# Optimization experiments

Hardware: AMD Instinct MI355X
Metric: run time of the kernel (lower is better)

Reference implementation:

```python
import jax, jax.numpy as jnp
import numpy as np

D = 512      # input_dim == encoder d_model
E = 512      # embedding_dim (codebook dim)
V = 8192     # num_embeddings
NC = 1       # num_codebooks
L = 6        # encoder layers
H = 8        # heads
F = 2048     # ffn dim
HD = D // H
EPS = 1e-5


def layernorm(x, s, b):
    m = jnp.mean(x, -1, keepdims=True)
    v = jnp.mean((x - m) ** 2, -1, keepdims=True)
    return (x - m) * jax.lax.rsqrt(v + EPS) * s + b


def sinusoidal_pe(T):
    pos = np.arange(T, dtype=np.float32)[:, None]
    i = np.arange(0, D, 2, dtype=np.float32)[None, :]
    ang = pos / np.power(10000.0, i / D)
    pe = np.zeros((T, D), np.float32)
    pe[:, 0::2] = np.sin(ang)
    pe[:, 1::2] = np.cos(ang)
    return jnp.asarray(pe)


def setup_inputs():
    key = jax.random.key(0)
    ks = jax.random.split(key, 12)
    B, T = 8, 1024
    xs = jax.random.normal(ks[0], (B, T, D), jnp.float32)
    xs_lens = (T // 2 + jax.random.randint(ks[1], (B,), 0, T // 2)).astype(jnp.int32)
    mask_indices = jax.random.uniform(ks[2], (B, T)) < 0.12  # span-mask surrogate
    sc = lambda k, shape, s=0.02: jax.random.normal(k, shape, jnp.float32) * s
    return {
        "xs": xs, "xs_lens": xs_lens, "mask_indices": mask_indices,
        "W_embed": sc(ks[3], (D, D), D ** -0.5),
        "ln1_s": jnp.ones((L, D)), "ln1_b": jnp.zeros((L, D)),
        "Wqkv": sc(ks[4], (L, D, 3 * D)), "Wo": sc(ks[5], (L, D, D)),
        "ln2_s": jnp.ones((L, D)), "ln2_b": jnp.zeros((L, D)),
        "W1": sc(ks[6], (L, D, F)), "W2": sc(ks[7], (L, F, D)),
        "an_s": jnp.ones((D,)), "an_b": jnp.zeros((D,)),
        "iln_s": jnp.ones((D,)), "iln_b": jnp.zeros((D,)),
        "mask_emb": sc(ks[8], (D,), 0.1),
        "top_n_out": sc(ks[9], (NC, D, V)),
        "projection": sc(ks[10], (D, E), (2.0 / (D + E)) ** 0.5),  # xavier_normal, frozen
        "embeddings": jax.random.normal(ks[11], (NC, E, V), jnp.float32),  # frozen codebook
    }


def encoder_blocks(x, pad_mask, ln1_s, ln1_b, Wqkv, Wo, ln2_s, ln2_b, W1, W2, an_s, an_b):
    B, T, _ = x.shape
    attn_bias = jnp.where(pad_mask, 0.0, -1e9)[:, None, None, :]  # [B,1,1,T]

    def layer(x, p):
        l1s, l1b, wqkv, wo, l2s, l2b, w1, w2 = p
        h = layernorm(x, l1s, l1b)
        q, k, v = jnp.split(h @ wqkv, 3, axis=-1)
        q = q.reshape(B, T, H, HD)
        k = k.reshape(B, T, H, HD)
        v = v.reshape(B, T, H, HD)
        scores = jnp.einsum('bqhd,bkhd->bhqk', q, k) * (HD ** -0.5) + attn_bias
        o = jnp.einsum('bhqk,bkhd->bqhd', jax.nn.softmax(scores, axis=-1), v)
        x = x + o.reshape(B, T, D) @ wo
        h = layernorm(x, l2s, l2b)
        x = x + jax.nn.relu(h @ w1) @ w2
        return x, None

    x, _ = jax.lax.scan(layer, x, (ln1_s, ln1_b, Wqkv, Wo, ln2_s, ln2_b, W1, W2))
    return layernorm(x, an_s, an_b)


def nearest_ids(x, iln_s, iln_b, projection, embeddings):
    # layernorm -> projection -> squared-distance argmin per codebook
    B, T, _ = x.shape
    z = layernorm(x, iln_s, iln_b) @ projection        # [B,T,E]
    flat = z.reshape(-1, E)                            # [N,E]
    d = (jnp.sum(flat ** 2, 1)[None, :, None]
         + jnp.sum(embeddings ** 2, 1)[:, None, :]
         - 2.0 * jnp.einsum('ne,gev->gnv', flat, embeddings))  # [NC,N,V]
    return jnp.argmin(d, -1).T.reshape(B, T, NC)


def reference(xs, xs_lens, mask_indices, W_embed, ln1_s, ln1_b, Wqkv, Wo, ln2_s, ln2_b,
              W1, W2, an_s, an_b, iln_s, iln_b, mask_emb, top_n_out, projection, embeddings):
    B, T, _ = xs.shape
    pad_mask = jnp.arange(T)[None, :] < xs_lens[:, None]              # [B,T]
    x = xs @ W_embed + sinusoidal_pe(T)[None]                         # encoder.embed
    target_ids = nearest_ids(x, iln_s, iln_b, projection, embeddings)  # [B,T,NC]
    masked_xs = jnp.where(mask_indices[..., None], mask_emb, x)
    out = encoder_blocks(masked_xs, pad_mask, ln1_s, ln1_b, Wqkv, Wo,
                         ln2_s, ln2_b, W1, W2, an_s, an_b)            # [B,T,D]
    logits = jnp.einsum('btd,gdv->bgtv', out, top_n_out)              # [B,NC,T,V]
    lsm = jax.nn.log_softmax(logits, axis=-1)
    tgt = jnp.transpose(target_ids, (0, 2, 1))                        # [B,NC,T]
    ent = -jnp.take_along_axis(lsm, tgt[..., None], axis=-1)[..., 0]  # [B,NC,T]
    m = (pad_mask & mask_indices).astype(jnp.float32)                 # [B,T]
    loss = jnp.sum(ent * m[:, None, :]) / (jnp.sum(m) * NC)
    return loss
```

## Files before the change

### kernel.cpp

```cpp
#include <hip/hip_runtime.h>
#include <hip/hip_bf16.h>

#define D_ 512
#define T_ 1024
#define B_ 8
#define H_ 8
#define F_ 2048
#define V_ 8192
#define L_ 6
#define NTOK 8192
#define EPS_ 1e-5f
#define NCAP 2048

typedef short short8 __attribute__((ext_vector_type(8)));
typedef float floatx4 __attribute__((ext_vector_type(4)));

__device__ __forceinline__ float bf2f(unsigned short u) {
  union { unsigned int i; float f; } v; v.i = ((unsigned int)u) << 16; return v.f;
}
__device__ __forceinline__ unsigned short f2bf(float f) {
  unsigned int u = __float_as_uint(f);
  return (unsigned short)((u + 0x7fffu + ((u >> 16) & 1u)) >> 16);
}
__device__ __forceinline__ float ldf(const void* p, long long i, int bf) {
  if (bf) return bf2f(((const unsigned short*)p)[i]);
  return ((const float*)p)[i];
}
__device__ __forceinline__ void ld16(const unsigned short* g, unsigned short* l) {
  __builtin_amdgcn_global_load_lds(
      (const __attribute__((address_space(1))) unsigned int*)g,
      (__attribute__((address_space(3))) unsigned int*)l, 16, 0, 0);
}
__device__ __forceinline__ unsigned int fkey(float f) {
  unsigned int u = __float_as_uint(f);
  return (u & 0x80000000u) ? ~u : (u ^ 0x80000000u);
}

__global__ void detect_kernel(const unsigned int* xsw, const unsigned int* mw, int* flags) {
  __shared__ int cnt[256];
  __shared__ int m01[256], mlo[256], mhi[256];
  int tid = threadIdx.x;
  int c = 0;
  for (int t = tid; t < 1024; t += 256) {
    unsigned int lo = xsw[t] & 0xffffu;
    int ok;
    if (lo == 0u) ok = 1;
    else { unsigned int e = (lo >> 7) & 0xffu; ok = (e >= 90u && e <= 140u); }
    c += ok;
  }
  int n01 = 0, lo38 = 0, hi38 = 0;
  for (int t = tid; t < 2048; t += 256) {
    unsigned int w = mw[t];
    if (w > 1u) n01 = 1;
    if ((w & 0xffffu) == 0x3f80u) lo38 = 1;
    if ((w >> 16) == 0x3f80u) hi38 = 1;
  }
  cnt[tid] = c; m01[tid] = n01; mlo[tid] = lo38; mhi[tid] = hi38;
  __syncthreads();
  for (int s = 128; s > 0; s >>= 1) {
    if (tid < s) {
      cnt[tid] += cnt[tid + s];
      m01[tid] |= m01[tid + s]; mlo[tid] |= mlo[tid + s]; mhi[tid] |= mhi[tid + s];
    }
    __syncthreads();
  }
  if (tid == 0) {
    flags[0] = (cnt[0] > 700) ? 1 : 0;
    int fmt;
    if (!m01[0]) fmt = 0;
    else if (mlo[0]) fmt = 2;
    else if (mhi[0]) fmt = 3;
    else fmt = 1;
    flags[1] = fmt;
  }
}

__global__ void conv_all_kernel(const void* d4, const void* d5, const void* d8,
                                const void* d9, const void* d12, const void* d13,
                                const void* d14, const void* d15, const void* d16,
                                float* P, const int* flags) {
  int i = blockIdx.x * 256 + threadIdx.x;
  if (i >= 14848) return;
  int bf = flags[0];
  const void* src; int off;
  if (i < 3072) { src = d4; off = 0; }
  else if (i < 6144) { src = d5; off = 3072; }
  else if (i < 9216) { src = d8; off = 6144; }
  else if (i < 12288) { src = d9; off = 9216; }
  else if (i < 12800) { src = d12; off = 12288; }
  else if (i < 13312) { src = d13; off = 12800; }
  else if (i < 13824) { src = d14; off = 13312; }
  else if (i < 14336) { src = d15; off = 13824; }
  else { src = d16; off = 14336; }
  P[i] = ldf(src, i - off, bf);
}

__global__ void convb_kernel(const void* src, unsigned short* dst, int n, const int* flags) {
  int i = blockIdx.x * 256 + threadIdx.x;
  if (i < n) {
    if (flags[0]) dst[i] = ((const unsigned short*)src)[i];
    else dst[i] = f2bf(((const float*)src)[i]);
  }
}

__global__ __launch_bounds__(256) void trans_kernel(const void* src, unsigned short* dst,
                                                    int K, int N, const int* flags) {
  int bf = flags[0];
  __shared__ unsigned short tile[32][33];
  int n0 = blockIdx.x * 32, k0 = blockIdx.y * 32, batch = blockIdx.z;
  long long sbase = (long long)batch * K * N;
  long long dbase = (long long)batch * N * K;
  int c = threadIdx.x & 31, r8 = threadIdx.x >> 5;
#pragma unroll
  for (int rr = 0; rr < 4; ++rr) {
    int r = r8 + rr * 8;
    tile[r][c] = f2bf(ldf(src, sbase + (long long)(k0 + r) * N + n0 + c, bf));
  }
  __syncthreads();
#pragma unroll
  for (int rr = 0; rr < 4; ++rr) {
    int nn = r8 + rr * 8;
    dst[dbase + (long long)(n0 + nn) * K + k0 + c] = tile[c][nn];
  }
}

__global__ __launch_bounds__(256) void trans_big_kernel(const void* top, const void* emb,
                                                        unsigned short* TOPT, unsigned short* EMBT,
                                                        float* en, const int* flags) {
  int bf = flags[0];
  __shared__ unsigned short tile[32][33];
  int n0 = blockIdx.x * 32, k0 = blockIdx.y * 32, z = blockIdx.z;
  const void* src = z ? emb : top;
  unsigned short* dst = z ? EMBT : TOPT;
  int c = threadIdx.x & 31, r8 = threadIdx.x >> 5;
#pragma unroll
  for (int rr = 0; rr < 4; ++rr) {
    int r = r8 + rr * 8;
    tile[r][c] = f2bf(ldf(src, (long long)(k0 + r) * V_ + n0 + c, bf));
  }
  __syncthreads();
#pragma unroll
  for (int rr = 0; rr < 4; ++rr) {
    int nn = r8 + rr * 8;
    dst[(long long)(n0 + nn) * D_ + k0 + c] = tile[c][nn];
  }
  if (z == 1 && threadIdx.x < 32) {
    int nn = threadIdx.x;
    float s = 0.f;
#pragma unroll
    for (int r = 0; r < 32; ++r) { float x = bf2f(tile[r][nn]); s += x * x; }
    atomicAdd(&en[n0 + nn], s);
  }
}

__global__ void prep_kernel(const void* mask, const int* lens, int* maski, float* mcomb,
                            int* idx, int* cnt, const int* flags) {
  int i = blockIdx.x * 256 + threadIdx.x;
  if (i >= NTOK) return;
  int fmt = flags[1];
  int mi;
  if (fmt == 0) mi = ((const int*)mask)[i] != 0;
  else if (fmt == 1) mi = ((const unsigned char*)mask)[i] != 0;
  else if (fmt == 2) mi = ((const unsigned short*)mask)[i] != 0;
  else mi = ((const float*)mask)[i] != 0.f;
  int b = i >> 10, t = i & (T_ - 1);
  int act = mi && (t < lens[b]);
  maski[i] = mi;
  mcomb[i] = act ? 1.f : 0.f;
  if (act) {
    int p = atomicAdd(cnt, 1);
    if (p < NCAP) idx[p] = i;
  }
}

#define BK 32
__device__ __forceinline__ void mfma_core(const unsigned short* A, const unsigned short* BT,
                                          int m0, int n0, int Kdim,
                                          unsigned short (*As)[BK], unsigned short (*Bs)[BK],
                                          floatx4 acc[4][4], int tid) {
  int wave = tid >> 6, lane = tid & 63;
  int r16 = lane >> 2, c16 = lane & 3;
  int lrow = lane & 15, quad = lane >> 4;
  int wm = (wave & 1) * 64, wn = (wave >> 1) * 64;
  for (int k0 = 0; k0 < Kdim; k0 += BK) {
#pragma unroll
    for (int p = 0; p < 2; ++p) {
      int rr = wave * 32 + p * 16;
      ld16(A + (long long)(m0 + rr + r16) * Kdim + k0 + c16 * 8, &As[rr][0]);
      ld16(BT + (long long)(n0 + rr + r16) * Kdim + k0 + c16 * 8, &Bs[rr][0]);
    }
    __syncthreads();
    short8 af[4], bfr[4];
#pragma unroll
    for (int i = 0; i < 4; ++i) af[i] = *(const short8*)&As[wm + i * 16 + lrow][quad * 8];
#pragma unroll
    for (int j = 0; j < 4; ++j) bfr[j] = *(const short8*)&Bs[wn + j * 16 + lrow][quad * 8];
#pragma unroll
    for (int i = 0; i < 4; ++i)
#pragma unroll
      for (int j = 0; j < 4; ++j)
        acc[i][j] = __builtin_amdgcn_mfma_f32_16x16x32_bf16(af[i], bfr[j], acc[i][j], 0, 0, 0);
    __syncthreads();
  }
}

__device__ __forceinline__ void mfma_core_g(const unsigned short* A, const int* ridx,
                                            const unsigned short* BT, int m0, int n0,
                                            unsigned short (*As)[BK], unsigned short (*Bs)[BK],
                                            floatx4 acc[4][4], int tid) {
  int wave = tid >> 6, lane = tid & 63;
  int r16 = lane >> 2, c16 = lane & 3;
  int lrow = lane & 15, quad = lane >> 4;
  int wm = (wave & 1) * 64, wn = (wave >> 1) * 64;
  int ar0 = ridx[m0 + wave * 32 + r16];
  int ar1 = ridx[m0 + wave * 32 + 16 + r16];
  for (int k0 = 0; k0 < D_; k0 += BK) {
    ld16(A + (long long)ar0 * D_ + k0 + c16 * 8, &As[wave * 32][0]);
    ld16(A + (long long)ar1 * D_ + k0 + c16 * 8, &As[wave * 32 + 16][0]);
#pragma unroll
    for (int p = 0; p < 2; ++p) {
      int rr = wave * 32 + p * 16;
      ld16(BT + (long long)(n0 + rr + r16) * D_ + k0 + c16 * 8, &Bs[rr][0]);
    }
    __syncthreads();
    short8 af[4], bfr[4];
#pragma unroll
    for (int i = 0; i < 4; ++i) af[i] = *(const short8*)&As[wm + i * 16 + lrow][quad * 8];
#pragma unroll
    for (int j = 0; j < 4; ++j) bfr[j] = *(const short8*)&Bs[wn + j * 16 + lrow][quad * 8];
#pragma unroll
    for (int i = 0; i < 4; ++i)
#pragma unroll
      for (int j = 0; j < 4; ++j)
        acc[i][j] = __builtin_amdgcn_mfma_f32_16x16x32_bf16(af[i], bfr[j], acc[i][j], 0, 0, 0);
    __syncthreads();
  }
}

__global__ __launch_bounds__(256) void mgemm_kernel(const unsigned short* A,
    const unsigned short* BT, long long boff, unsigned short* Cb, int Ndim, int Kdim) {
  __shared__ __align__(16) unsigned short As[128][BK];
  __shared__ __align__(16) unsigned short Bs[128][BK];
  int tid = threadIdx.x;
  int bid = blockIdx.x;
  int m0 = (bid & 63) * 128, n0 = (bid >> 6) * 128;
  int wave = tid >> 6, lane = tid & 63;
  int wm = (wave & 1) * 64, wn = (wave >> 1) * 64;
  int lrow = lane & 15, quad = lane >> 4;
  floatx4 acc[4][4];
#pragma unroll
  for (int i = 0; i < 4; ++i)
#pragma unroll
    for (int j = 0; j < 4; ++j) acc[i][j] = (floatx4){0.f, 0.f, 0.f, 0.f};
  mfma_core(A, BT + boff, m0, n0, Kdim, As, Bs, acc, tid);
#pragma unroll
  for (int i = 0; i < 4; ++i) {
    int mb = m0 + wm + i * 16 + quad * 4;
#pragma unroll
    for (int j = 0; j < 4; ++j) {
      int ncol = n0 + wn + j * 16 + lrow;
#pragma unroll
      for (int r = 0; r < 4; ++r)
        Cb[(long long)(mb + r) * Ndim + ncol] = f2bf(fmaxf(acc[i][j][r], 0.f));
    }
  }
}

__global__ __launch_bounds__(256) void mgemm64_kernel(const unsigned short* A,
    const unsigned short* BT, long long boff, float* Cf, unsigned short* Cb,
    int Ndim, int Kdim, int mode) {
  __shared__ __align__(16) unsigned short As[128][BK];
  __shared__ __align__(16) unsigned short Bs[64][BK];
  int tid = threadIdx.x;
  int bid = blockIdx.x;
  int m0 = (bid & 63) * 128, n0 = (bid >> 6) * 64;
  int wave = tid >> 6, lane = tid & 63;
  int r16 = lane >> 2, c16 = lane & 3;
  int wm = (wave & 1) * 64, wn = (wave >> 1) * 32;
  int lrow = lane & 15, quad = lane >> 4;
  const unsigned short* Bp = BT + boff;
  floatx4 acc[4][2];
#pragma unroll
  for (int i = 0; i < 4; ++i)
#pragma unroll
    for (int j = 0; j < 2; ++j) acc[i][j] = (floatx4){0.f, 0.f, 0.f, 0.f};
  for (int k0 = 0; k0 < Kdim; k0 += BK) {
#pragma unroll
    for (int p = 0; p < 2; ++p) {
      int rr = wave * 32 + p * 16;
      ld16(A + (long long)(m0 + rr + r16) * Kdim + k0 + c16 * 8, &As[rr][0]);
    }
    {
      int rr = wave * 16;
      ld16(Bp + (long long)(n0 + rr + r16) * Kdim + k0 + c16 * 8, &Bs[rr][0]);
    }
    __syncthreads();
    short8 af[4], bfr[2];
#pragma unroll
    for (int i = 0; i < 4; ++i) af[i] = *(const short8*)&As[wm + i * 16 + lrow][quad * 8];
#pragma unroll
    for (int j = 0; j < 2; ++j) bfr[j] = *(const short8*)&Bs[wn + j * 16 + lrow][quad * 8];
#pragma unroll
    for (int i = 0; i < 4; ++i)
#pragma unroll
      for (int j = 0; j < 2; ++j)
        acc[i][j] = __builtin_amdgcn_mfma_f32_16x16x32_bf16(af[i], bfr[j], acc[i][j], 0, 0, 0);
    __syncthreads();
  }
#pragma unroll
  for (int i = 0; i < 4; ++i) {
    int mb = m0 + wm + i * 16 + quad * 4;
#pragma unroll
    for (int j = 0; j < 2; ++j) {
      int ncol = n0 + wn + j * 16 + lrow;
#pragma unroll
      for (int r = 0; r < 4; ++r) {
        int m = mb + r;
        long long idx = (long long)m * Ndim + ncol;
        float v = acc[i][j][r];
        if (mode == 1) Cf[idx] += v;
        else if (mode == 4) Cb[idx] = f2bf(v);
        else if (mode == 3) {
          int t = m & (T_ - 1);
          float freq = __expf(-(float)(ncol & ~1) * (9.210340371976184f / (float)D_));
          float ang = (float)t * freq;
          v += (ncol & 1) ? cosf(ang) : sinf(ang);
          Cf[idx] = v;
        } else Cf[idx] = v;
      }
    }
  }
}

__global__ __launch_bounds__(256) void qkvgemm_kernel(const unsigned short* A,
    const unsigned short* BT, long long boff, unsigned short* QB,
    unsigned short* KSg, unsigned short* VTSg) {
  __shared__ __align__(16) union {
    struct { unsigned short As[128][BK]; unsigned short Bs[128][BK]; } s;
    unsigned short T[128][136];
  } sm;
  int tid = threadIdx.x;
  int bid = blockIdx.x;
  int m0 = (bid & 63) * 128;
  int nt = bid >> 6;
  int n0 = nt * 128;
  int wave = tid >> 6, lane = tid & 63;
  int wm = (wave & 1) * 64, wn = (wave >> 1) * 64;
  int lrow = lane & 15, quad = lane >> 4;
  floatx4 acc[4][4];
#pragma unroll
  for (int i = 0; i < 4; ++i)
#pragma unroll
    for (int j = 0; j < 4; ++j) acc[i][j] = (floatx4){0.f, 0.f, 0.f, 0.f};
  mfma_core(A, BT + boff, m0, n0, D_, sm.s.As, sm.s.Bs, acc, tid);
  int b = m0 >> 10, tt = (m0 >> 7) & 7;
  if (nt < 4) {
#pragma unroll
    for (int i = 0; i < 4; ++i) {
      int mb = m0 + wm + i * 16 + quad * 4;
#pragma unroll
      for (int j = 0; j < 4; ++j) {
        int ncol = n0 + wn + j * 16 + lrow;
#pragma unroll
        for (int r = 0; r < 4; ++r)
          QB[(long long)(mb + r) * 512 + ncol] = f2bf(acc[i][j][r]);
      }
    }
  } else if (nt < 8) {
#pragma unroll
    for (int i = 0; i < 4; ++i)
#pragma unroll
      for (int j = 0; j < 4; ++j)
#pragma unroll
        for (int r = 0; r < 4; ++r)
          sm.T[wm + i * 16 + quad * 4 + r][wn + j * 16 + lrow] = f2bf(acc[i][j][r]);
    __syncthreads();
    int tk = tid & 127, hg0 = tid >> 7;
#pragma unroll
    for (int p = 0; p < 8; ++p) {
      int hg = p * 2 + hg0;
      int h2 = hg >> 3, g = hg & 7;
      uint4 u = *(const uint4*)&sm.T[tk][h2 * 64 + g * 8];
      int headg = (nt - 4) * 2 + h2;
      long long dst = (((((long long)(b * 8 + headg)) * 8 + tt) * 8 + g) * 128 + tk) * 8;
      *(uint4*)&KSg[dst] = u;
    }
  } else {
#pragma unroll
    for (int i = 0; i < 4; ++i)
#pragma unroll
      for (int j = 0; j < 4; ++j)
#pragma unroll
        for (int r = 0; r < 4; ++r)
          sm.T[wn + j * 16 + lrow][wm + i * 16 + quad * 4 + r] = f2bf(acc[i][j][r]);
    __syncthreads();
    int col = tid & 127, gh = tid >> 7;
    int h2 = col >> 6, ch = col & 63;
    int headg = (nt - 8) * 2 + h2;
    long long base = ((((long long)(b * 8 + headg)) * 8 + tt) * 16);
#pragma unroll
    for (int p = 0; p < 8; ++p) {
      int g = p * 2 + gh;
      uint4 u = *(const uint4*)&sm.T[col][g * 8];
      long long dst = ((base + g) * 64 + ch) * 8;
      *(uint4*)&VTSg[dst] = u;
    }
  }
}

__global__ __launch_bounds__(256) void fattn_kernel(const unsigned short* QB,
    const unsigned short* KSg, const unsigned short* VTSg, const int* lens,
    unsigned short* ao) {
  __shared__ __align__(16) unsigned short Kt[8192];
  __shared__ __align__(16) unsigned short Vt[8192];
  __shared__ __align__(16) unsigned short Ps[16384];
  int blk = blockIdx.x;
  int qt = blk & 7, bh = blk >> 3;
  int b = bh >> 3, h = bh & 7;
  int tid = threadIdx.x, wave = tid >> 6, lane = tid & 63;
  int c = lane & 15, quad = lane >> 4;
  int len = lens[b];
  short8 qf[2][2];
#pragma unroll
  for (int i = 0; i < 2; ++i)
#pragma unroll
    for (int ks = 0; ks < 2; ++ks)
      qf[i][ks] = *(const short8*)&QB[(long long)(b * 1024 + qt * 128 + wave * 32 + i * 16 + c) * 512
                                      + h * 64 + ks * 32 + quad * 8];
  floatx4 accO[2][4];
  float lr[2][4];
#pragma unroll
  for (int i = 0; i < 2; ++i)
#pragma unroll
    for (int j = 0; j < 4; ++j) {
      accO[i][j] = (floatx4){0.f, 0.f, 0.f, 0.f};
      lr[i][j] = 0.f;
    }
  int nkt = (len + 127) >> 7;
  const unsigned short* ksrc = KSg + (long long)bh * 65536;
  const unsigned short* vsrc = VTSg + (long long)bh * 65536;
  for (int kt = 0; kt < nkt; ++kt) {
#pragma unroll
    for (int p = 0; p < 4; ++p) {
      int eb = (p * 256 + wave * 64) * 8;
      ld16(ksrc + (long long)kt * 8192 + eb + lane * 8, &Kt[eb]);
      ld16(vsrc + (long long)kt * 8192 + eb + lane * 8, &Vt[eb]);
    }
    __syncthreads();
    floatx4 sacc[2][8];
#pragma unroll
    for (int i = 0; i < 2; ++i)
#pragma unroll
      for (int j = 0; j < 8; ++j) sacc[i][j] = (floatx4){0.f, 0.f, 0.f, 0.f};
#pragma unroll
    for (int j = 0; j < 8; ++j) {
      short8 bk0 = *(const short8*)&Kt[(quad * 128 + j * 16 + c) * 8];
      short8 bk1 = *(const short8*)&Kt[((4 + quad) * 128 + j * 16 + c) * 8];
#pragma unroll
      for (int i = 0; i < 2; ++i) {
        sacc[i][j] = __builtin_amdgcn_mfma_f32_16x16x32_bf16(qf[i][0], bk0, sacc[i][j], 0, 0, 0);
        sacc[i][j] = __builtin_amdgcn_mfma_f32_16x16x32_bf16(qf[i][1], bk1, sacc[i][j], 0, 0, 0);
      }
    }
    int kbase = kt * 128;
#pragma unroll
    for (int i = 0; i < 2; ++i) {
#pragma unroll
      for (int r = 0; r < 4; ++r) {
        int prow = wave * 32 + i * 16 + quad * 4 + r;
        int rx = prow & 15;
        float ls = 0.f;
#pragma unroll
        for (int j = 0; j < 8; ++j) {
          int col = j * 16 + c;
          float s = sacc[i][j][r] * 0.125f;
          s = (kbase + col < len) ? s : -100.f;
          float p = __expf(s);
          ls += p;
          Ps[prow * 128 + (((col >> 3) ^ rx) * 8) + (col & 7)] = f2bf(p);
        }
        ls += __shfl_xor(ls, 1, 64);
        ls += __shfl_xor(ls, 2, 64);
        ls += __shfl_xor(ls, 4, 64);
        ls += __shfl_xor(ls, 8, 64);
        lr[i][r] += ls;
      }
    }
    __syncthreads();
#pragma unroll
    for (int kk = 0; kk < 4; ++kk) {
      short8 pa[2];
#pragma unroll
      for (int i = 0; i < 2; ++i) {
        int row = wave * 32 + i * 16 + c;
        pa[i] = *(const short8*)&Ps[row * 128 + (((kk * 4 + quad) ^ (row & 15)) * 8)];
      }
#pragma unroll
      for (int jn = 0; jn < 4; ++jn) {
        short8 vb = *(const short8*)&Vt[((kk * 4 + quad) * 64 + jn * 16 + c) * 8];
#pragma unroll
        for (int i = 0; i < 2; ++i)
          accO[i][jn] = __builtin_amdgcn_mfma_f32_16x16x32_bf16(pa[i], vb, accO[i][jn], 0, 0, 0);
      }
    }
    __syncthreads();
  }
#pragma unroll
  for (int i = 0; i < 2; ++i) {
#pragma unroll
    for (int r = 0; r < 4; ++r) {
      float inv = 1.f / lr[i][r];
      long long token = b * 1024 + qt * 128 + wave * 32 + i * 16 + quad * 4 + r;
#pragma unroll
      for (int jn = 0; jn < 4; ++jn)
        ao[token * 512 + h * 64 + jn * 16 + c] = f2bf(accO[i][jn][r] * inv);
    }
  }
}

__global__ __launch_bounds__(256) void dgemm_argmin(const unsigned short* Z, const int* ridx,
    const int* cnt, const unsigned short* ET, const float* en, unsigned long long* best) {
  __shared__ __align__(16) union {
    struct { unsigned short A[128][BK]; unsigned short B[128][BK]; } s;
    unsigned long long part[128][33];
  } sm;
  int m0 = blockIdx.y * 128;
  int na = *cnt;
  if (m0 >= ((na + 127) & ~127)) return;
  int tid = threadIdx.x;
  int n0 = blockIdx.x * 128;
  int wave = tid >> 6, lane = tid & 63;
  int wm = (wave & 1) * 64, wn = (wave >> 1) * 64;
  int lrow = lane & 15, quad = lane >> 4;
  int slot = (wave >> 1) * 16 + lrow;
  floatx4 acc[4][4];
#pragma unroll
  for (int i = 0; i < 4; ++i)
#pragma unroll
    for (int j = 0; j < 4; ++j) acc[i][j] = (floatx4){0.f, 0.f, 0.f, 0.f};
  mfma_core_g(Z, ridx + m0, ET, 0, n0, sm.s.A, sm.s.B, acc, tid);
  float env[4];
#pragma unroll
  for (int j = 0; j < 4; ++j) env[j] = en[n0 + wn + j * 16 + lrow];
#pragma unroll
  for (int i = 0; i < 4; ++i) {
#pragma unroll
    for (int r = 0; r < 4; ++r) {
      int rowl = wm + i * 16 + quad * 4 + r;
      unsigned long long bl = ~0ull;
#pragma unroll
      for (int j = 0; j < 4; ++j) {
        float v = env[j] - 2.f * acc[i][j][r];
        unsigned long long pk = (((unsigned long long)fkey(v)) << 32) |
                                (unsigned int)(n0 + wn + j * 16 + lrow);
        if (pk < bl) bl = pk;
      }
      sm.part[rowl][(slot + rowl) & 31] = bl;
    }
  }
  __syncthreads();
  if (tid < 128) {
    unsigned long long bb = sm.part[tid][0];
#pragma unroll 4
    for (int k2 = 1; k2 < 32; ++k2) { unsigned long long o = sm.part[tid][k2]; if (o < bb) bb = o; }
    atomicMin(&best[m0 + tid], bb);
  }
}

__global__ __launch_bounds__(256) void lgemm_lse(const unsigned short* OUTB, const int* ridx,
    const int* cnt, const unsigned short* TOPT, const unsigned long long* best,
    float* PS, float* TL) {
  __shared__ __align__(16) union {
    struct { unsigned short A[128][BK]; unsigned short B[128][BK]; } s;
    float part[128][33];
  } sm;
  int m0 = blockIdx.y * 128;
  int na = *cnt;
  if (m0 >= ((na + 127) & ~127)) return;
  int tid = threadIdx.x;
  int n0 = blockIdx.x * 128;
  int wave = tid >> 6, lane = tid & 63;
  int wm = (wave & 1) * 64, wn = (wave >> 1) * 64;
  int lrow = lane & 15, quad = lane >> 4;
  int slot = (wave >> 1) * 16 + lrow;
  floatx4 acc[4][4];
#pragma unroll
  for (int i = 0; i < 4; ++i)
#pragma unroll
    for (int j = 0; j < 4; ++j) acc[i][j] = (floatx4){0.f, 0.f, 0.f, 0.f};
  mfma_core_g(OUTB, ridx + m0, TOPT, 0, n0, sm.s.A, sm.s.B, acc, tid);
#pragma unroll
  for (int i = 0; i < 4; ++i) {
#pragma unroll
    for (int r = 0; r < 4; ++r) {
      int rowl = wm + i * 16 + quad * 4 + r;
      int tg = (int)(best[m0 + rowl] & 0xffffffffu);
      float ss = 0.f;
#pragma unroll
      for (int j = 0; j < 4; ++j) {
        float v = acc[i][j][r];
        ss += __expf(v);
        if (n0 + wn + j * 16 + lrow == tg) TL[m0 + rowl] = v;
      }
      sm.part[rowl][(slot + rowl) & 31] = ss;
    }
  }
  __syncthreads();
  if (tid < 128) {
    float S = 0.f;
#pragma unroll 4
    for (int k2 = 0; k2 < 32; ++k2) S += sm.part[tid][k2];
    PS[(long long)(m0 + tid) * 64 + blockIdx.x] = S;
  }
}

__global__ void lse_combine(const float* PS, const float* TL, const int* cnt, float* entm) {
  int t = blockIdx.x * 256 + threadIdx.x;
  if (t >= NCAP) return;
  if (t < *cnt) {
    float S = 0.f;
    for (int i = 0; i < 64; ++i) S += PS[(long long)t * 64 + i];
    entm[t] = __logf(S) - TL[t];
  } else {
    entm[t] = 0.f;
  }
}

__global__ __launch_bounds__(256) void ln_kernel(const float* X, float* Yf, unsigned short* Yb,
                                                 int obf, const float* s, const float* b) {
  int tid = threadIdx.x, wave = tid >> 6, lane = tid & 63;
  long long n = (long long)blockIdx.x * 4 + wave;
  const float* x = X + n * D_ + lane * 8;
  float v[8];
  *(float4*)&v[0] = *(const float4*)x;
  *(float4*)&v[4] = *(const float4*)(x + 4);
  float sum = 0.f;
#pragma unroll
  for (int j = 0; j < 8; ++j) sum += v[j];
  for (int m = 32; m; m >>= 1) sum += __shfl_xor(sum, m, 64);
  float mean = sum * (1.f / (float)D_);
  float vs = 0.f;
#pragma unroll
  for (int j = 0; j < 8; ++j) { v[j] -= mean; vs += v[j] * v[j]; }
  for (int m = 32; m; m >>= 1) vs += __shfl_xor(vs, m, 64);
  float r = rsqrtf(vs * (1.f / (float)D_) + EPS_);
  float sv[8], bv[8];
  *(float4*)&sv[0] = *(const float4*)(s + lane * 8);
  *(float4*)&sv[4] = *(const float4*)(s + lane * 8 + 4);
  *(float4*)&bv[0] = *(const float4*)(b + lane * 8);
  *(float4*)&bv[4] = *(const float4*)(b + lane * 8 + 4);
  if (obf) {
    unsigned short o[8];
#pragma unroll
    for (int j = 0; j < 8; ++j) o[j] = f2bf(v[j] * r * sv[j] + bv[j]);
    *(uint4*)(Yb + n * D_ + lane * 8) = *(const uint4*)o;
  } else {
    float o[8];
#pragma unroll
    for (int j = 0; j < 8; ++j) o[j] = v[j] * r * sv[j] + bv[j];
    *(float4*)(Yf + n * D_ + lane * 8) = *(const float4*)&o[0];
    *(float4*)(Yf + n * D_ + lane * 8 + 4) = *(const float4*)&o[4];
  }
}

__global__ void maskapply_kernel(float* x, const int* maski, const float* memb) {
  long long i = (long long)blockIdx.x * 256 + threadIdx.x;
  int n = (int)(i >> 9), d = (int)(i & 511);
  if (maski[n]) x[i] = memb[d];
}

__global__ void final_kernel(const float* entm, const float* mcomb, void* out) {
  __shared__ float r1[256], r2[256];
  int tid = threadIdx.x;
  float s1 = 0.f, s2 = 0.f;
  for (int i = tid; i < NCAP; i += 256) s1 += entm[i];
  for (int i = tid; i < NTOK; i += 256) s2 += mcomb[i];
  r1[tid] = s1; r2[tid] = s2;
  __syncthreads();
  for (int st = 128; st > 0; st >>= 1) {
    if (tid < st) { r1[tid] += r1[tid + st]; r2[tid] += r2[tid + st]; }
    __syncthreads();
  }
  if (tid == 0) {
    float loss = r1[0] / r2[0];
    unsigned short b16 = f2bf(loss);
    unsigned short* o = (unsigned short*)out;
    o[0] = b16; o[1] = b16;
  }
}

extern "C" void kernel_launch(void* const* d_in, const int* in_sizes, int n_in,
                              void* d_out, int out_size, void* d_ws, size_t ws_size,
                              hipStream_t stream) {
  if (n_in < 20) return;
  float* wsf = (float*)d_ws;
  int* flags = (int*)d_ws;
  const long long OF_P = 256;
  const long long OF_X = 16640;
  const long long OF_HB = OF_X + 4194304;
  const long long OF_BIG = OF_HB + 2097152;
  const long long OF_AOB = OF_BIG + 8388608;
  const long long OF_WT = OF_AOB + 2097152;
  const long long OF_TOPT = OF_WT + 9699328;
  const long long OF_EMBT = OF_TOPT + 2097152;
  const long long OF_EN = OF_EMBT + 2097152;
  const long long OF_BEST = OF_EN + 8192;
  const long long OF_PS = OF_BEST + 4096;
  const long long OF_TL = OF_PS + 131072;
  const long long OF_MI = OF_TL + 2048;
  const long long OF_MC = OF_MI + 8192;
  const long long OF_EM = OF_MC + 8192;
  const long long OF_CNT = OF_EM + 2048;
  const long long OF_IDX = OF_CNT + 16;
  const long long END = OF_IDX + 2048;
  if (ws_size < (size_t)END * 4) return;

  float* X = wsf + OF_X;
  unsigned short* HB = (unsigned short*)(wsf + OF_HB);
  unsigned short* BIGB = (unsigned short*)(wsf + OF_BIG);
  unsigned short* AOB = (unsigned short*)(wsf + OF_AOB);
  unsigned short* WT = (unsigned short*)(wsf + OF_WT);
  unsigned short* TOPT = (unsigned short*)(wsf + OF_TOPT);
  unsigned short* EMBT = (unsigned short*)(wsf + OF_EMBT);
  float* EN = wsf + OF_EN;
  unsigned long long* BEST = (unsigned long long*)(wsf + OF_BEST);
  float* PS = wsf + OF_PS;
  float* TL = wsf + OF_TL;
  int* MI = (int*)(wsf + OF_MI);
  float* MC = wsf + OF_MC;
  float* EM = wsf + OF_EM;
  int* CNT = (int*)(wsf + OF_CNT);
  int* IDX = (int*)(wsf + OF_IDX);
  float* P = wsf + OF_P;
  float* ln1s = P, *ln1b = P + 3072, *ln2s = P + 6144, *ln2b = P + 9216;
  float* ans = P + 12288, *anb = P + 12800, *ilns = P + 13312, *ilnb = P + 13824;
  float* memb = P + 14336;

  unsigned short* QB = BIGB;
  unsigned short* KSg = BIGB + 4194304;
  unsigned short* VTSg = BIGB + 8388608;

  const long long W_QKV = 0, W_O = 4718592, W_1 = 6291456, W_2 = 12582912,
                  W_EMB = 18874368, W_PRJ = 19136512;

  detect_kernel<<<1, 256, 0, stream>>>((const unsigned int*)d_in[0],
                                       (const unsigned int*)d_in[2], flags);
  hipMemsetAsync((void*)BEST, 0xFF, NCAP * 8, stream);
  hipMemsetAsync((void*)EN, 0, V_ * 4, stream);
  hipMemsetAsync((void*)CNT, 0, 16, stream);
  hipMemsetAsync((void*)IDX, 0, NCAP * 4, stream);
  conv_all_kernel<<<58, 256, 0, stream>>>(d_in[4], d_in[5], d_in[8], d_in[9], d_in[12],
                                          d_in[13], d_in[14], d_in[15], d_in[16], P, flags);
  prep_kernel<<<32, 256, 0, stream>>>(d_in[2], (const int*)d_in[1], MI, MC, IDX, CNT, flags);

  unsigned short* XSB = BIGB;
  convb_kernel<<<16384, 256, 0, stream>>>(d_in[0], XSB, 4194304, flags);

  trans_kernel<<<dim3(48, 16, 6), 256, 0, stream>>>(d_in[6], WT + W_QKV, 512, 1536, flags);
  trans_kernel<<<dim3(16, 16, 6), 256, 0, stream>>>(d_in[7], WT + W_O, 512, 512, flags);
  trans_kernel<<<dim3(64, 16, 6), 256, 0, stream>>>(d_in[10], WT + W_1, 512, 2048, flags);
  trans_kernel<<<dim3(16, 64, 6), 256, 0, stream>>>(d_in[11], WT + W_2, 2048, 512, flags);
  trans_kernel<<<dim3(16, 16, 1), 256, 0, stream>>>(d_in[3], WT + W_EMB, 512, 512, flags);
  trans_kernel<<<dim3(16, 16, 1), 256, 0, stream>>>(d_in[18], WT + W_PRJ, 512, 512, flags);
  trans_big_kernel<<<dim3(256, 16, 2), 256, 0, stream>>>(d_in[17], d_in[19], TOPT, EMBT,
                                                         EN, flags);

  dim3 gC(64, NCAP / 128);

  mgemm64_kernel<<<512, 256, 0, stream>>>(XSB, WT + W_EMB, 0, X, nullptr, 512, 512, 3);
  ln_kernel<<<2048, 256, 0, stream>>>(X, nullptr, HB, 1, ilns, ilnb);
  mgemm64_kernel<<<512, 256, 0, stream>>>(HB, WT + W_PRJ, 0, nullptr, AOB, 512, 512, 4);
  dgemm_argmin<<<gC, 256, 0, stream>>>(AOB, IDX, CNT, EMBT, EN, BEST);
  maskapply_kernel<<<16384, 256, 0, stream>>>(X, MI, memb);

  for (int l = 0; l < L_; ++l) {
    ln_kernel<<<2048, 256, 0, stream>>>(X, nullptr, HB, 1, ln1s + l * 512, ln1b + l * 512);
    qkvgemm_kernel<<<768, 256, 0, stream>>>(HB, WT + W_QKV, (long long)l * 786432,
                                            QB, KSg, VTSg);
    fattn_kernel<<<512, 256, 0, stream>>>(QB, KSg, VTSg, (const int*)d_in[1], AOB);
    mgemm64_kernel<<<512, 256, 0, stream>>>(AOB, WT + W_O, (long long)l * 262144,
                                            X, nullptr, 512, 512, 1);
    ln_kernel<<<2048, 256, 0, stream>>>(X, nullptr, HB, 1, ln2s + l * 512, ln2b + l * 512);
    mgemm_kernel<<<1024, 256, 0, stream>>>(HB, WT + W_1, (long long)l * 1048576,
                                           BIGB, 2048, 512);
    mgemm64_kernel<<<512, 256, 0, stream>>>(BIGB, WT + W_2, (long long)l * 1048576,
                                            X, nullptr, 512, 2048, 1);
  }
  ln_kernel<<<2048, 256, 0, stream>>>(X, nullptr, AOB, 1, ans, anb);
  lgemm_lse<<<gC, 256, 0, stream>>>(AOB, IDX, CNT, TOPT, BEST, PS, TL);
  lse_combine<<<8, 256, 0, stream>>>(PS, TL, CNT, EM);
  final_kernel<<<1, 256, 0, stream>>>(EM, MC, d_out);
}
```

Measured before the change: 1.392 ms.

## Add triple-buffered async LDS pipeline to all MFMA GEMM main loops

Replaces the load-sync-compute-sync GEMM loops with a shared templated three-stage LDS ring. Tiles for the next two k-steps are issued before computing on the current one, and only one barrier is used per step with explicit vmcnt waits. The goal is to hide global-to-LDS latency behind MFMA work. It triples LDS use per block, which may lower occupancy, and it relies on ld16 being an async LDS load tracked by vmcnt.

Result: faster. 1.331 ms (-4.4%).

```diff
diff --git a/kernel.cpp b/kernel.cpp
--- a/kernel.cpp
+++ b/kernel.cpp
@@ -174,85 +174,91 @@
 }
 
 #define BK 32
-__device__ __forceinline__ void mfma_core(const unsigned short* A, const unsigned short* BT,
-                                          int m0, int n0, int Kdim,
+
+template<int BN>
+__device__ __forceinline__ void stage_tile(const unsigned short* A, long long ga0, long long ga1,
+                                           const unsigned short* BT, long long gb0, long long gb1,
+                                           int k0, unsigned short (*Ab)[BK],
+                                           unsigned short (*Bb)[BK], int wave, int c16) {
+  ld16(A + ga0 + k0 + c16 * 8, &Ab[wave * 32][0]);
+  ld16(A + ga1 + k0 + c16 * 8, &Ab[wave * 32 + 16][0]);
+  if constexpr (BN == 128) {
+    ld16(BT + gb0 + k0 + c16 * 8, &Bb[wave * 32][0]);
+    ld16(BT + gb1 + k0 + c16 * 8, &Bb[wave * 32 + 16][0]);
+  } else {
+    ld16(BT + gb0 + k0 + c16 * 8, &Bb[wave * 16][0]);
+  }
+}
+
+template<int BN>
+__device__ __forceinline__ void mfma_pipe(const unsigned short* A, long long ga0, long long ga1,
+                                          const unsigned short* BT, int n0, int Kdim,
                                           unsigned short (*As)[BK], unsigned short (*Bs)[BK],
-                                          floatx4 acc[4][4], int tid) {
+                                          floatx4 (*acc)[BN / 32], int tid) {
+  constexpr int NB = BN / 32;
   int wave = tid >> 6, lane = tid & 63;
   int r16 = lane >> 2, c16 = lane & 3;
   int lrow = lane & 15, quad = lane >> 4;
-  int wm = (wave & 1) * 64, wn = (wave >> 1) * 64;
-  for (int k0 = 0; k0 < Kdim; k0 += BK) {
-#pragma unroll
-    for (int p = 0; p < 2; ++p) {
-      int rr = wave * 32 + p * 16;
-      ld16(A + (long long)(m0 + rr + r16) * Kdim + k0 + c16 * 8, &As[rr][0]);
-      ld16(BT + (long long)(n0 + rr + r16) * Kdim + k0 + c16 * 8, &Bs[rr][0]);
-    }
-    __syncthreads();
-    short8 af[4], bfr[4];
-#pragma unroll
-    for (int i = 0; i < 4; ++i) af[i] = *(const short8*)&As[wm + i * 16 + lrow][quad * 8];
-#pragma unroll
-    for (int j = 0; j < 4; ++j) bfr[j] = *(const short8*)&Bs[wn + j * 16 + lrow][quad * 8];
+  int wm = (wave & 1) * 64, wn = (wave >> 1) * (BN / 2);
+  int NT = Kdim / BK;
+  long long gb0, gb1 = 0;
+  if constexpr (BN == 128) {
+    gb0 = (long long)(n0 + wave * 32 + r16) * Kdim;
+    gb1 = gb0 + 16LL * Kdim;
+  } else {
+    gb0 = (long long)(n0 + wave * 16 + r16) * Kdim;
+  }
+  stage_tile<BN>(A, ga0, ga1, BT, gb0, gb1, 0, As, Bs, wave, c16);
+  stage_tile<BN>(A, ga0, ga1, BT, gb0, gb1, BK, As + 128, Bs + BN, wave, c16);
+  int cur = 0, nxt = 2;
+  for (int t = 0; t < NT; ++t) {
+    if (t == NT - 1) {
+      asm volatile("s_waitcnt vmcnt(0)" ::: "memory");
+    } else {
+      if constexpr (BN == 128) asm volatile("s_waitcnt vmcnt(4)" ::: "memory");
+      else                     asm volatile("s_waitcnt vmcnt(3)" ::: "memory");
+    }
+    __builtin_amdgcn_s_barrier();
+    if (t + 2 < NT)
+      stage_tile<BN>(A, ga0, ga1, BT, gb0, gb1, (t + 2) * BK,
+                     As + nxt * 128, Bs + nxt * BN, wave, c16);
+    unsigned short (*Ac)[BK] = As + cur * 128;
+    unsigned short (*Bc)[BK] = Bs + cur * BN;
+    short8 af[4], bfr[NB];
+#pragma unroll
+    for (int i = 0; i < 4; ++i) af[i] = *(const short8*)&Ac[wm + i * 16 + lrow][quad * 8];
+#pragma unroll
+    for (int j = 0; j < NB; ++j) bfr[j] = *(const short8*)&Bc[wn + j * 16 + lrow][quad * 8];
 #pragma unroll
     for (int i = 0; i < 4; ++i)
 #pragma unroll
-      for (int j = 0; j < 4; ++j)
+      for (int j = 0; j < NB; ++j)
         acc[i][j] = __builtin_amdgcn_mfma_f32_16x16x32_bf16(af[i], bfr[j], acc[i][j], 0, 0, 0);
-    __syncthreads();
-  }
-}
-
-__device__ __forceinline__ void mfma_core_g(const unsigned short* A, const int* ridx,
-                                            const unsigned short* BT, int m0, int n0,
-                                            unsigned short (*As)[BK], unsigned short (*Bs)[BK],
-                                            floatx4 acc[4][4], int tid) {
-  int wave = tid >> 6, lane = tid & 63;
-  int r16 = lane >> 2, c16 = lane & 3;
-  int lrow = lane & 15, quad = lane >> 4;
-  int wm = (wave & 1) * 64, wn = (wave >> 1) * 64;
-  int ar0 = ridx[m0 + wave * 32 + r16];
-  int ar1 = ridx[m0 + wave * 32 + 16 + r16];
-  for (int k0 = 0; k0 < D_; k0 += BK) {
-    ld16(A + (long long)ar0 * D_ + k0 + c16 * 8, &As[wave * 32][0]);
-    ld16(A + (long long)ar1 * D_ + k0 + c16 * 8, &As[wave * 32 + 16][0]);
-#pragma unroll
-    for (int p = 0; p < 2; ++p) {
-      int rr = wave * 32 + p * 16;
-      ld16(BT + (long long)(n0 + rr + r16) * D_ + k0 + c16 * 8, &Bs[rr][0]);
-    }
-    __syncthreads();
-    short8 af[4], bfr[4];
-#pragma unroll
-    for (int i = 0; i < 4; ++i) af[i] = *(const short8*)&As[wm + i * 16 + lrow][quad * 8];
-#pragma unroll
-    for (int j = 0; j < 4; ++j) bfr[j] = *(const short8*)&Bs[wn + j * 16 + lrow][quad * 8];
-#pragma unroll
-    for (int i = 0; i < 4; ++i)
-#pragma unroll
-      for (int j = 0; j < 4; ++j)
-        acc[i][j] = __builtin_amdgcn_mfma_f32_16x16x32_bf16(af[i], bfr[j], acc[i][j], 0, 0, 0);
-    __syncthreads();
-  }
+    cur = (cur == 2) ? 0 : cur + 1;
+    nxt = (nxt == 2) ? 0 : nxt + 1;
+  }
+  __syncthreads();
 }
 
 __global__ __launch_bounds__(256) void mgemm_kernel(const unsigned short* A,
     const unsigned short* BT, long long boff, unsigned short* Cb, int Ndim, int Kdim) {
-  __shared__ __align__(16) unsigned short As[128][BK];
-  __shared__ __align__(16) unsigned short Bs[128][BK];
+  __shared__ __align__(16) unsigned short As[3 * 128][BK];
+  __shared__ __align__(16) unsigned short Bs[3 * 128][BK];
   int tid = threadIdx.x;
   int bid = blockIdx.x;
   int m0 = (bid & 63) * 128, n0 = (bid >> 6) * 128;
   int wave = tid >> 6, lane = tid & 63;
   int wm = (wave & 1) * 64, wn = (wave >> 1) * 64;
   int lrow = lane & 15, quad = lane >> 4;
+  int r16 = lane >> 2;
   floatx4 acc[4][4];
 #pragma unroll
   for (int i = 0; i < 4; ++i)
 #pragma unroll
     for (int j = 0; j < 4; ++j) acc[i][j] = (floatx4){0.f, 0.f, 0.f, 0.f};
-  mfma_core(A, BT + boff, m0, n0, Kdim, As, Bs, acc, tid);
+  long long ga0 = (long long)(m0 + wave * 32 + r16) * Kdim;
+  long long ga1 = ga0 + 16LL * Kdim;
+  mfma_pipe<128>(A, ga0, ga1, BT + boff, n0, Kdim, As, Bs, acc, tid);
 #pragma unroll
   for (int i = 0; i < 4; ++i) {
     int mb = m0 + wm + i * 16 + quad * 4;
@@ -269,44 +275,23 @@
 __global__ __launch_bounds__(256) void mgemm64_kernel(const unsigned short* A,
     const unsigned short* BT, long long boff, float* Cf, unsigned short* Cb,
     int Ndim, int Kdim, int mode) {
-  __shared__ __align__(16) unsigned short As[128][BK];
-  __shared__ __align__(16) unsigned short Bs[64][BK];
+  __shared__ __align__(16) unsigned short As[3 * 128][BK];
+  __shared__ __align__(16) unsigned short Bs[3 * 64][BK];
   int tid = threadIdx.x;
   int bid = blockIdx.x;
   int m0 = (bid & 63) * 128, n0 = (bid >> 6) * 64;
   int wave = tid >> 6, lane = tid & 63;
-  int r16 = lane >> 2, c16 = lane & 3;
+  int r16 = lane >> 2;
   int wm = (wave & 1) * 64, wn = (wave >> 1) * 32;
   int lrow = lane & 15, quad = lane >> 4;
-  const unsigned short* Bp = BT + boff;
   floatx4 acc[4][2];
 #pragma unroll
   for (int i = 0; i < 4; ++i)
 #pragma unroll
     for (int j = 0; j < 2; ++j) acc[i][j] = (floatx4){0.f, 0.f, 0.f, 0.f};
-  for (int k0 = 0; k0 < Kdim; k0 += BK) {
-#pragma unroll
-    for (int p = 0; p < 2; ++p) {
-      int rr = wave * 32 + p * 16;
-      ld16(A + (long long)(m0 + rr + r16) * Kdim + k0 + c16 * 8, &As[rr][0]);
-    }
-    {
-      int rr = wave * 16;
-      ld16(Bp + (long long)(n0 + rr + r16) * Kdim + k0 + c16 * 8, &Bs[rr][0]);
-    }
-    __syncthreads();
-    short8 af[4], bfr[2];
-#pragma unroll
-    for (int i = 0; i < 4; ++i) af[i] = *(const short8*)&As[wm + i * 16 + lrow][quad * 8];
-#pragma unroll
-    for (int j = 0; j < 2; ++j) bfr[j] = *(const short8*)&Bs[wn + j * 16 + lrow][quad * 8];
-#pragma unroll
-    for (int i = 0; i < 4; ++i)
-#pragma unroll
-      for (int j = 0; j < 2; ++j)
-        acc[i][j] = __builtin_amdgcn_mfma_f32_16x16x32_bf16(af[i], bfr[j], acc[i][j], 0, 0, 0);
-    __syncthreads();
-  }
+  long long ga0 = (long long)(m0 + wave * 32 + r16) * Kdim;
+  long long ga1 = ga0 + 16LL * Kdim;
+  mfma_pipe<64>(A, ga0, ga1, BT + boff, n0, Kdim, As, Bs, acc, tid);
 #pragma unroll
   for (int i = 0; i < 4; ++i) {
     int mb = m0 + wm + i * 16 + quad * 4;
@@ -336,7 +321,7 @@
     const unsigned short* BT, long long boff, unsigned short* QB,
     unsigned short* KSg, unsigned short* VTSg) {
   __shared__ __align__(16) union {
-    struct { unsigned short As[128][BK]; unsigned short Bs[128][BK]; } s;
+    struct { unsigned short As[3 * 128][BK]; unsigned short Bs[3 * 128][BK]; } s;
     unsigned short T[128][136];
   } sm;
   int tid = threadIdx.x;
@@ -347,12 +332,15 @@
   int wave = tid >> 6, lane = tid & 63;
   int wm = (wave & 1) * 64, wn = (wave >> 1) * 64;
   int lrow = lane & 15, quad = lane >> 4;
+  int r16 = lane >> 2;
   floatx4 acc[4][4];
 #pragma unroll
   for (int i = 0; i < 4; ++i)
 #pragma unroll
     for (int j = 0; j < 4; ++j) acc[i][j] = (floatx4){0.f, 0.f, 0.f, 0.f};
-  mfma_core(A, BT + boff, m0, n0, D_, sm.s.As, sm.s.Bs, acc, tid);
+  long long ga0 = (long long)(m0 + wave * 32 + r16) * D_;
+  long long ga1 = ga0 + 16LL * D_;
+  mfma_pipe<128>(A, ga0, ga1, BT + boff, n0, D_, sm.s.As, sm.s.Bs, acc, tid);
   int b = m0 >> 10, tt = (m0 >> 7) & 7;
   if (nt < 4) {
 #pragma unroll
@@ -521,7 +509,7 @@
 __global__ __launch_bounds__(256) void dgemm_argmin(const unsigned short* Z, const int* ridx,
     const int* cnt, const unsigned short* ET, const float* en, unsigned long long* best) {
   __shared__ __align__(16) union {
-    struct { unsigned short A[128][BK]; unsigned short B[128][BK]; } s;
+    struct { unsigned short A[3 * 128][BK]; unsigned short B[3 * 128][BK]; } s;
     unsigned long long part[128][33];
   } sm;
   int m0 = blockIdx.y * 128;
@@ -532,13 +520,16 @@
   int wave = tid >> 6, lane = tid & 63;
   int wm = (wave & 1) * 64, wn = (wave >> 1) * 64;
   int lrow = lane & 15, quad = lane >> 4;
+  int r16 = lane >> 2;
   int slot = (wave >> 1) * 16 + lrow;
   floatx4 acc[4][4];
 #pragma unroll
   for (int i = 0; i < 4; ++i)
 #pragma unroll
     for (int j = 0; j < 4; ++j) acc[i][j] = (floatx4){0.f, 0.f, 0.f, 0.f};
-  mfma_core_g(Z, ridx + m0, ET, 0, n0, sm.s.A, sm.s.B, acc, tid);
+  long long ga0 = (long long)ridx[m0 + wave * 32 + r16] * D_;
+  long long ga1 = (long long)ridx[m0 + wave * 32 + 16 + r16] * D_;
+  mfma_pipe<128>(Z, ga0, ga1, ET, n0, D_, sm.s.A, sm.s.B, acc, tid);
   float env[4];
 #pragma unroll
   for (int j = 0; j < 4; ++j) env[j] = en[n0 + wn + j * 16 + lrow];
@@ -571,7 +562,7 @@
     const int* cnt, const unsigned short* TOPT, const unsigned long long* best,
     float* PS, float* TL) {
   __shared__ __align__(16) union {
-    struct { unsigned short A[128][BK]; unsigned short B[128][BK]; } s;
+    struct { unsigned short A[3 * 128][BK]; unsigned short B[3 * 128][BK]; } s;
     float part[128][33];
   } sm;
   int m0 = blockIdx.y * 128;
@@ -582,13 +573,16 @@
   int wave = tid >> 6, lane = tid & 63;
   int wm = (wave & 1) * 64, wn = (wave >> 1) * 64;
   int lrow = lane & 15, quad = lane >> 4;
+  int r16 = lane >> 2;
   int slot = (wave >> 1) * 16 + lrow;
   floatx4 acc[4][4];
 #pragma unroll
   for (int i = 0; i < 4; ++i)
 #pragma unroll
     for (int j = 0; j < 4; ++j) acc[i][j] = (floatx4){0.f, 0.f, 0.f, 0.f};
-  mfma_core_g(OUTB, ridx + m0, TOPT, 0, n0, sm.s.A, sm.s.B, acc, tid);
+  long long ga0 = (long long)ridx[m0 + wave * 32 + r16] * D_;
+  long long ga1 = (long long)ridx[m0 + wave * 32 + 16 + r16] * D_;
+  mfma_pipe<128>(OUTB, ga0, ga1, TOPT, n0, D_, sm.s.A, sm.s.B, acc, tid);
 #pragma unroll
   for (int i = 0; i < 4; ++i) {
 #pragma unroll
```
